# Optimization experiments

Hardware: AMD Instinct MI355X
Metric: run time of the kernel (lower is better)

## Reference

```python
import jax, jax.numpy as jnp
import numpy as np

B, L, D, N = 8, 1024, 1024, 32  # N = d_state // 2 (complex conjugate-pair modes)
DT_MIN, DT_MAX = 0.001, 0.1


def setup_inputs() -> dict:
    key = jax.random.key(0)
    ks = jax.random.split(key, 12)
    s = 1.0 / np.sqrt(D)  # torch Linear / Conv1d default init bound
    inp = {
        "x": jax.random.normal(ks[0], (B, L, D), jnp.float32),
        "in_W": jax.random.uniform(ks[1], (D, D), jnp.float32, -s, s),
        "in_b": jax.random.uniform(ks[2], (D,), jnp.float32, -s, s),
        # S4D kernel params
        "log_dt": (np.log(DT_MIN)
                   + jax.random.uniform(ks[3], (D,), jnp.float32)
                   * (np.log(DT_MAX) - np.log(DT_MIN))).astype(jnp.float32),
        "C": jax.random.normal(ks[4], (D, N, 2), jnp.float32),  # complex C as (re, im)
        "log_A_real": jnp.log(0.5 * jnp.ones((D, N), jnp.float32)),
        "A_imag": jnp.tile((np.pi * jnp.arange(N, dtype=np.float32))[None, :], (D, 1)),
        "D_skip": jax.random.normal(ks[5], (D,), jnp.float32),
        # output_linear = Conv1d(D, 2D, 1) + GLU(dim=-2); kernel squeezed to (2D, D)
        "glu_W": jax.random.uniform(ks[6], (2 * D, D), jnp.float32, -s, s),
        "glu_b": jax.random.uniform(ks[7], (2 * D,), jnp.float32, -s, s),
        "out_W": jax.random.uniform(ks[8], (D, D), jnp.float32, -s, s),
        "out_b": jax.random.uniform(ks[9], (D,), jnp.float32, -s, s),
    }
    return inp


def reference(x, in_W, in_b, log_dt, C, log_A_real, A_imag, D_skip,
              glu_W, glu_b, out_W, out_b):
    # in_proj
    x_in = x @ in_W.T + in_b                      # (B, L, D)
    u = jnp.swapaxes(x_in, 1, 2)                  # (B, D, L) -- transposed=False path
    Lseq = u.shape[-1]

    # ---- S4D kernel (ZOH-like discretization of diagonal SSM) ----
    dt = jnp.exp(log_dt)                          # (D,)
    Cc = (C[..., 0] + 1j * C[..., 1]).astype(jnp.complex64)   # (D, N)
    A = (-jnp.exp(log_A_real) + 1j * A_imag).astype(jnp.complex64)
    dtA = A * dt[:, None].astype(jnp.complex64)   # (D, N)
    # Vandermonde: exp(dtA * l) for l in [0, L)
    K = jnp.exp(dtA[:, :, None] * jnp.arange(Lseq, dtype=jnp.float32))  # (D, N, L)
    Ceff = Cc * (jnp.exp(dtA) - 1.0) / A
    k = 2.0 * jnp.einsum('hn,hnl->hl', Ceff, K).real            # (D, L)

    # ---- FFT causal convolution ----
    n = 2 * Lseq
    k_f = jnp.fft.rfft(k, n=n)                    # (D, L+1)
    u_f = jnp.fft.rfft(u, n=n)                    # (B, D, L+1)
    y = jnp.fft.irfft(u_f * k_f, n=n)[..., :Lseq] # (B, D, L)

    y = y + u * D_skip[:, None]                   # skip connection
    y = jax.nn.gelu(y, approximate=False)         # torch nn.GELU (erf)

    # Conv1d(D, 2D, kernel=1) + GLU over channel dim
    z = jnp.einsum('oh,bhl->bol', glu_W, y) + glu_b[None, :, None]
    a, g = jnp.split(z, 2, axis=1)
    y = a * jax.nn.sigmoid(g)                     # (B, D, L)

    y = jnp.swapaxes(y, 1, 2)                     # (B, L, D)
    out = y @ out_W.T + out_b
    return out + x
```

## Files before the change

### kernel.cpp

```cpp
#include <hip/hip_runtime.h>
#include <math.h>

#define BB 8
#define LL 1024
#define DD 1024
#define KD 1024
#define NM 32
#define NCH 16
#define CL 64
#define NTOK (BB * LL)
#define GSMEM 147456

typedef __bf16 bf16_t;
typedef __bf16 bf16x8 __attribute__((ext_vector_type(8)));
typedef __bf16 bf16x4 __attribute__((ext_vector_type(4)));
typedef float  f32x4  __attribute__((ext_vector_type(4)));

__device__ __forceinline__ float gelu_f(float z)
{
    float t = fmaf(0.044715f * z * z, z, z);
    return z / (1.f + expf(-1.5957691216f * t));
}

__global__ __launch_bounds__(256)
void f2b_all_kernel(const float* __restrict__ x,    bf16_t* __restrict__ xb,
                    const float* __restrict__ w0,   bf16_t* __restrict__ d0,
                    const float* __restrict__ w1,   bf16_t* __restrict__ d1,
                    const float* __restrict__ w2,   bf16_t* __restrict__ d2)
{
    int b = blockIdx.x;
    const float* s; bf16_t* d; int base;
    if (b < 8192)       { s = x;  d = xb; base = b; }
    else if (b < 9216)  { s = w0; d = d0; base = b - 8192; }
    else if (b < 11264) { s = w1; d = d1; base = b - 9216; }
    else                { s = w2; d = d2; base = b - 11264; }
    int i = (base * 256 + threadIdx.x) * 4;
    float4 f = *(const float4*)(s + i);
    bf16x4 o = { (bf16_t)f.x, (bf16_t)f.y, (bf16_t)f.z, (bf16_t)f.w };
    *(bf16x4*)(d + i) = o;
}

__device__ __forceinline__ void stage_tile(const bf16_t* __restrict__ Ag,
                                           const bf16_t* __restrict__ Bg,
                                           bf16_t* Asb, bf16_t* Bsb, int tid)
{
    #pragma unroll
    for (int p = 0; p < 4; ++p) {
        int e = p * 512 + tid;
        int row = e >> 3, c8 = (e & 7) << 3;
        int sc = c8 ^ ((row & 7) << 3);
        __builtin_amdgcn_global_load_lds(
            (const __attribute__((address_space(1))) void*)(Ag + (size_t)row * KD + sc),
            (__attribute__((address_space(3))) void*)(Asb + e * 8), 16, 0, 0);
    }
    #pragma unroll
    for (int p = 0; p < 2; ++p) {
        int e = p * 512 + tid;
        int row = e >> 3, c8 = (e & 7) << 3;
        int sc = c8 ^ ((row & 7) << 3);
        __builtin_amdgcn_global_load_lds(
            (const __attribute__((address_space(1))) void*)(Bg + (size_t)row * KD + sc),
            (__attribute__((address_space(3))) void*)(Bsb + e * 8), 16, 0, 0);
    }
}

__device__ __forceinline__ void compute_tile(const bf16_t* Asb, const bf16_t* Bsb,
                                             int wy, int wx, int lm, int ks,
                                             f32x4 (&acc)[4][4])
{
    #pragma unroll
    for (int kk = 0; kk < 2; ++kk) {
        bf16x8 af[4], bfr[4];
        const int col = kk * 32 + ks;
        #pragma unroll
        for (int i = 0; i < 4; ++i) {
            int row = wy * 64 + i * 16 + lm;
            af[i] = *(const bf16x8*)(Asb + row * 64 + (col ^ ((row & 7) << 3)));
        }
        #pragma unroll
        for (int j = 0; j < 4; ++j) {
            int row = wx * 64 + j * 16 + lm;
            bfr[j] = *(const bf16x8*)(Bsb + row * 64 + (col ^ ((row & 7) << 3)));
        }
        __builtin_amdgcn_s_setprio(1);
        #pragma unroll
        for (int i = 0; i < 4; ++i)
            #pragma unroll
            for (int j = 0; j < 4; ++j)
                acc[i][j] = __builtin_amdgcn_mfma_f32_16x16x32_bf16(
                                af[i], bfr[j], acc[i][j], 0, 0, 0);
        __builtin_amdgcn_s_setprio(0);
    }
}

template<int MODE>
__global__ __launch_bounds__(512, 2)
void gemm3_kernel(const bf16_t* __restrict__ A, const bf16_t* __restrict__ B,
                  const float* __restrict__ bias, const float* __restrict__ res,
                  void* __restrict__ outp)
{
    extern __shared__ __align__(16) bf16_t lds[];
    bf16_t* As0 = lds;
    bf16_t* Bs0 = lds + 3 * 16384;

    const int tid = threadIdx.x;
    const int lane = tid & 63, w = tid >> 6;
    const int wy = w >> 1, wx = w & 1;
    const int lm = lane & 15, ks = (lane >> 4) << 3;

    const int nbx = gridDim.x;
    int bid = blockIdx.y * nbx + blockIdx.x;
    const int cpx = (gridDim.x * gridDim.y) >> 3;
    bid = (bid & 7) * cpx + (bid >> 3);
    const int by = bid / nbx, bx = bid % nbx;
    const int m0 = by * 256, n0 = bx * 128;

    const bf16_t* Ag     = A + (size_t)m0 * KD;
    const bf16_t* Bbase0 = B + (size_t)n0 * KD;
    const bf16_t* Bbase1 = (MODE == 1) ? B + (size_t)(1024 + n0) * KD : Bbase0;
    const int NTT = (MODE == 1) ? 32 : 16;

    f32x4 acc[4][4]  = {};
    f32x4 acc2[4][4] = {};

    stage_tile(Ag,      Bbase0,      As0,         Bs0,        tid);
    stage_tile(Ag + 64, Bbase0 + 64, As0 + 16384, Bs0 + 8192, tid);
    asm volatile("s_waitcnt vmcnt(6)" ::: "memory");
    __builtin_amdgcn_s_barrier();

    #pragma unroll 1
    for (int t = 0; t < NTT; ++t) {
        if (t + 2 < NTT) {
            int q2 = (t + 2) % 3;
            const bf16_t* Agt = Ag + ((t + 2) & 15) * 64;
            const bf16_t* Bgt = ((MODE == 1 && t + 2 >= 16) ? Bbase1 : Bbase0)
                                + ((t + 2) & 15) * 64;
            stage_tile(Agt, Bgt, As0 + q2 * 16384, Bs0 + q2 * 8192, tid);
        }
        int q = t % 3;
        if (MODE == 1 && t >= 16)
            compute_tile(As0 + q * 16384, Bs0 + q * 8192, wy, wx, lm, ks, acc2);
        else
            compute_tile(As0 + q * 16384, Bs0 + q * 8192, wy, wx, lm, ks, acc);
        if (t + 1 < NTT) {
            if (t + 2 < NTT) asm volatile("s_waitcnt vmcnt(6) lgkmcnt(0)" ::: "memory");
            else             asm volatile("s_waitcnt vmcnt(0) lgkmcnt(0)" ::: "memory");
            __builtin_amdgcn_s_barrier();
        }
    }

    const int r4 = (lane >> 4) << 2;
    #pragma unroll
    for (int i = 0; i < 4; ++i)
        #pragma unroll
        for (int r = 0; r < 4; ++r) {
            int m = m0 + wy * 64 + i * 16 + r4 + r;
            #pragma unroll
            for (int j = 0; j < 4; ++j) {
                int n = n0 + wx * 64 + j * 16 + lm;
                if (MODE == 0) {
                    ((bf16_t*)outp)[(size_t)m * 8192 + n] =
                        (bf16_t)(acc[i][j][r] + bias[m]);
                } else if (MODE == 1) {
                    float a = acc[i][j][r]  + bias[n];
                    float g = acc2[i][j][r] + bias[1024 + n];
                    ((bf16_t*)outp)[(size_t)m * 1024 + n] =
                        (bf16_t)(a / (1.f + expf(-g)));
                } else {
                    ((float*)outp)[(size_t)m * 1024 + n] =
                        acc[i][j][r] + bias[n] + res[(size_t)m * 1024 + n];
                }
            }
        }
}

__global__ __launch_bounds__(64)
void genVTP_kernel(const float* __restrict__ log_dt, const float* __restrict__ lar,
                   const float* __restrict__ aim, const float* __restrict__ Cp,
                   const float* __restrict__ dskip,
                   bf16_t* __restrict__ V, bf16_t* __restrict__ TP)
{
    const int tid = threadIdx.x;
    if (blockIdx.x < DD / 2) {
        const int h = blockIdx.x * 2 + (tid >> 5);
        const int n = tid & 31;
        const float dt = expf(log_dt[h]);
        const float ardt = -expf(lar[h * NM + n]) * dt;
        const float aidt = aim[h * NM + n] * dt;
        float sn, cs;
        sincosf(aidt, &sn, &cs);
        float er = expf(ardt);
        float wr = er * cs, wi = er * sn;
        float inv = 1.f / fmaf(wr, wr, wi * wi);
        float vr = wr * inv, vi = -wi * inv;
        sincosf(63.f * aidt, &sn, &cs);
        er = expf(63.f * ardt);
        float pr = er * cs, pi = er * sn;
        bf16_t* rowr = V + ((size_t)h * 64 + 2 * n) * 64;
        bf16_t* rowi = rowr + 64;
        #pragma unroll
        for (int c8 = 0; c8 < 8; ++c8) {
            bf16x8 rr, ri;
            #pragma unroll
            for (int e = 0; e < 8; ++e) {
                rr[e] = (bf16_t)pr; ri[e] = (bf16_t)pi;
                float t = fmaf(pr, vr, -pi * vi);
                pi = fmaf(pr, vi, pi * vr);
                pr = t;
            }
            *(bf16x8*)(rowr + c8 * 8) = rr;
            *(bf16x8*)(rowi + c8 * 8) = ri;
        }
        return;
    }
    __shared__ float ardt_s[NM], aidt_s[NM], cr_s[NM], ci_s[NM], K_s[CL];
    const int h = blockIdx.x - DD / 2;
    const float dt = expf(log_dt[h]);
    if (tid < NM) {
        int n = tid;
        float ar = -expf(lar[h * NM + n]);
        float ai = aim[h * NM + n];
        float sn, cs;
        sincosf(ai * dt, &sn, &cs);
        float er = expf(ar * dt);
        float wrr = er * cs, wii = er * sn;
        float Crr = Cp[(h * NM + n) * 2 + 0];
        float Cii = Cp[(h * NM + n) * 2 + 1];
        float nr = fmaf(Crr, wrr - 1.f, -Cii * wii);
        float ni = fmaf(Crr, wii, Cii * (wrr - 1.f));
        float inv = 2.f / fmaf(ar, ar, ai * ai);
        cr_s[n] = fmaf(nr, ar, ni * ai) * inv;
        ci_s[n] = fmaf(ni, ar, -nr * ai) * inv;
        ardt_s[n] = ar * dt;
        aidt_s[n] = ai * dt;
    }
    __syncthreads();
    {
        float d = (float)tid;
        float kv = (tid == 0) ? dskip[h] : 0.f;
        #pragma unroll 8
        for (int n = 0; n < NM; ++n) {
            float sn, cs;
            sincosf(aidt_s[n] * d, &sn, &cs);
            float e = expf(ardt_s[n] * d);
            kv = fmaf(cr_s[n], e * cs, kv);
            kv = fmaf(-ci_s[n], e * sn, kv);
        }
        K_s[tid] = kv;
    }
    __syncthreads();
    const int i = tid;
    bf16_t* row = TP + ((size_t)h * CL + i) * 128;
    #pragma unroll
    for (int c8 = 0; c8 < 8; ++c8) {
        bf16x8 v;
        #pragma unroll
        for (int e = 0; e < 8; ++e) {
            int l = c8 * 8 + e;
            v[e] = (l <= i) ? (bf16_t)K_s[i - l] : (bf16_t)0.f;
        }
        *(bf16x8*)(row + c8 * 8) = v;
    }
    const float fi = (float)(i + 1);
    #pragma unroll
    for (int c8 = 0; c8 < 8; ++c8) {
        bf16x8 v;
        #pragma unroll
        for (int q = 0; q < 4; ++q) {
            int n = c8 * 4 + q;
            float sn, cs;
            sincosf(aidt_s[n] * fi, &sn, &cs);
            float e = expf(ardt_s[n] * fi);
            float Wr = e * cs, Wi = e * sn;
            v[2 * q]     = (bf16_t)(fmaf(cr_s[n], Wr, -ci_s[n] * Wi));
            v[2 * q + 1] = (bf16_t)(-fmaf(cr_s[n], Wi, ci_s[n] * Wr));
        }
        *(bf16x8*)(row + 64 + c8 * 8) = v;
    }
}

__global__ __launch_bounds__(256)
void ssm_fused_kernel(const bf16_t* __restrict__ u_ch, const bf16_t* __restrict__ V,
                      const bf16_t* __restrict__ TP,
                      const float* __restrict__ log_dt, const float* __restrict__ lar,
                      const float* __restrict__ aim, bf16_t* __restrict__ y_bi)
{
    __shared__ float  Sbc_s[128 * 64];
    __shared__ bf16_t Sc_s[128 * 64];
    const int h = blockIdx.x;
    const int tid = threadIdx.x;
    const int lane = tid & 63, w = tid >> 6;
    const int lm = lane & 15, ks = (lane >> 4) << 3;
    const bf16_t* U   = u_ch + (size_t)h * 8192;
    const bf16_t* Vh  = V    + (size_t)h * 4096;
    const bf16_t* TPh = TP   + (size_t)h * 8192;

    bf16x8 af_u[2][2];
    #pragma unroll
    for (int im = 0; im < 2; ++im)
        #pragma unroll
        for (int kk = 0; kk < 2; ++kk)
            af_u[im][kk] = *(const bf16x8*)(U + (((w << 1) + im) * 16 + lm) * 64
                                            + kk * 32 + ks);

    f32x4 acc1[2][4] = {};
    #pragma unroll
    for (int kk = 0; kk < 2; ++kk) {
        bf16x8 bfr[4];
        #pragma unroll
        for (int jn = 0; jn < 4; ++jn)
            bfr[jn] = *(const bf16x8*)(Vh + (jn * 16 + lm) * 64 + kk * 32 + ks);
        #pragma unroll
        for (int im = 0; im < 2; ++im)
            #pragma unroll
            for (int jn = 0; jn < 4; ++jn)
                acc1[im][jn] = __builtin_amdgcn_mfma_f32_16x16x32_bf16(
                                   af_u[im][kk], bfr[jn], acc1[im][jn], 0, 0, 0);
    }
    const int r4 = (lane >> 4) << 2;
    #pragma unroll
    for (int im = 0; im < 2; ++im)
        #pragma unroll
        for (int jn = 0; jn < 4; ++jn)
            #pragma unroll
            for (int r = 0; r < 4; ++r)
                Sbc_s[(((w << 1) + im) * 16 + r4 + r) * 64 + jn * 16 + lm]
                    = acc1[im][jn][r];
    __syncthreads();

    {
        const int b = tid >> 5, n = tid & 31;
        const float dtv = expf(log_dt[h]);
        const float ardt = -expf(lar[h * NM + n]) * dtv;
        const float aidt = aim[h * NM + n] * dtv;
        float sn, cs;
        sincosf(64.f * aidt, &sn, &cs);
        float er = expf(64.f * ardt);
        const float gr = er * cs, gi = er * sn;
        float sr = 0.f, si = 0.f;
        for (int c = 0; c < NCH; ++c) {
            int idx = (b * 16 + c) * 64 + 2 * n;
            float lr = Sbc_s[idx], li = Sbc_s[idx + 1];
            Sc_s[idx]     = (bf16_t)sr;
            Sc_s[idx + 1] = (bf16_t)si;
            float t0 = fmaf(gr, sr, fmaf(-gi, si, lr));
            si = fmaf(gr, si, fmaf(gi, sr, li));
            sr = t0;
        }
    }
    __syncthreads();

    f32x4 acc2[2][4] = {};
    #pragma unroll
    for (int kk = 0; kk < 4; ++kk) {
        bf16x8 af[2], bfr[4];
        #pragma unroll
        for (int im = 0; im < 2; ++im) {
            if (kk < 2)
                af[im] = af_u[im][kk];
            else
                af[im] = *(bf16x8*)&Sc_s[(((w << 1) + im) * 16 + lm) * 64
                                         + (kk - 2) * 32 + ks];
        }
        #pragma unroll
        for (int jn = 0; jn < 4; ++jn)
            bfr[jn] = *(const bf16x8*)(TPh + (jn * 16 + lm) * 128 + kk * 32 + ks);
        #pragma unroll
        for (int im = 0; im < 2; ++im)
            #pragma unroll
            for (int jn = 0; jn < 4; ++jn)
                acc2[im][jn] = __builtin_amdgcn_mfma_f32_16x16x32_bf16(
                                   af[im], bfr[jn], acc2[im][jn], 0, 0, 0);
    }
    bf16_t* out = y_bi + (size_t)h * 8192;
    #pragma unroll
    for (int im = 0; im < 2; ++im)
        #pragma unroll
        for (int jn = 0; jn < 4; ++jn)
            #pragma unroll
            for (int r = 0; r < 4; ++r) {
                int batch = ((w << 1) + im) * 16 + r4 + r;
                int i = jn * 16 + lm;
                out[batch * 64 + i] = (bf16_t)gelu_f(acc2[im][jn][r]);
            }
}

__global__ __launch_bounds__(256)
void transpose_kernel(const bf16_t* __restrict__ src, bf16_t* __restrict__ dst,
                      int src_rows, int src_cols)
{
    __shared__ unsigned short tile[64][68];
    const int tid = threadIdx.x;
    const int c0 = blockIdx.x << 6, r0 = blockIdx.y << 6;
    const int r = tid >> 4, c4 = (tid & 15) << 2;
    #pragma unroll
    for (int p = 0; p < 4; ++p) {
        int rr = p * 16 + r;
        ushort4 v = *(const ushort4*)((const unsigned short*)src +
                                      (size_t)(r0 + rr) * src_cols + c0 + c4);
        *(ushort4*)&tile[rr][c4] = v;
    }
    __syncthreads();
    #pragma unroll
    for (int p = 0; p < 4; ++p) {
        int rr = p * 16 + r;
        ushort4 v;
        v.x = tile[c4 + 0][rr];
        v.y = tile[c4 + 1][rr];
        v.z = tile[c4 + 2][rr];
        v.w = tile[c4 + 3][rr];
        *(ushort4*)((unsigned short*)dst + (size_t)(c0 + rr) * src_rows + r0 + c4) = v;
    }
}

extern "C" void kernel_launch(void* const* d_in, const int* in_sizes, int n_in,
                              void* d_out, int out_size, void* d_ws, size_t ws_size,
                              hipStream_t stream)
{
    (void)in_sizes; (void)n_in; (void)out_size; (void)ws_size;
    const float* x      = (const float*)d_in[0];
    const float* in_W   = (const float*)d_in[1];
    const float* in_b   = (const float*)d_in[2];
    const float* log_dt = (const float*)d_in[3];
    const float* Cp     = (const float*)d_in[4];
    const float* lar    = (const float*)d_in[5];
    const float* aim    = (const float*)d_in[6];
    const float* dsk    = (const float*)d_in[7];
    const float* gluW   = (const float*)d_in[8];
    const float* glub   = (const float*)d_in[9];
    const float* outW   = (const float*)d_in[10];
    const float* outb   = (const float*)d_in[11];

    char* ws = (char*)d_ws;
    bf16_t* xb    = (bf16_t*)(ws);
    bf16_t* TP    = (bf16_t*)(ws);
    bf16_t* y_tok = (bf16_t*)(ws);
    bf16_t* V     = (bf16_t*)(ws + 16777216);
    bf16_t* vb    = (bf16_t*)(ws + 16777216);
    bf16_t* u_ch  = (bf16_t*)(ws + 33554432);
    bf16_t* wbin  = (bf16_t*)(ws + 50331648);
    bf16_t* wbglu = (bf16_t*)(ws + 52428800);
    bf16_t* wbout = (bf16_t*)(ws + 56623104);
    bf16_t* y_bi  = (bf16_t*)d_out;

    static bool s_attr = false;
    if (!s_attr) {
        hipFuncSetAttribute((const void*)gemm3_kernel<0>,
                            hipFuncAttributeMaxDynamicSharedMemorySize, GSMEM);
        hipFuncSetAttribute((const void*)gemm3_kernel<1>,
                            hipFuncAttributeMaxDynamicSharedMemorySize, GSMEM);
        hipFuncSetAttribute((const void*)gemm3_kernel<2>,
                            hipFuncAttributeMaxDynamicSharedMemorySize, GSMEM);
        s_attr = true;
    }

    f2b_all_kernel<<<dim3(12288), dim3(256), 0, stream>>>(
        x, xb, in_W, wbin, gluW, wbglu, outW, wbout);

    gemm3_kernel<0><<<dim3(NTOK / 128, DD / 256), dim3(512), GSMEM, stream>>>(
        wbin, xb, in_b, nullptr, u_ch);

    genVTP_kernel<<<dim3(DD / 2 + DD), dim3(64), 0, stream>>>(
        log_dt, lar, aim, Cp, dsk, V, TP);
    ssm_fused_kernel<<<dim3(DD), dim3(256), 0, stream>>>(
        u_ch, V, TP, log_dt, lar, aim, y_bi);

    transpose_kernel<<<dim3(NTOK / 64, DD / 64), dim3(256), 0, stream>>>(y_bi, y_tok, DD, NTOK);
    gemm3_kernel<1><<<dim3(1024 / 128, NTOK / 256), dim3(512), GSMEM, stream>>>(
        y_tok, wbglu, glub, nullptr, vb);

    gemm3_kernel<2><<<dim3(DD / 128, NTOK / 256), dim3(512), GSMEM, stream>>>(
        vb, wbout, outb, x, d_out);
}
```

Before: 293.0 us.

## Interleave GEMM tile prefetch with MFMA phases using split barriers

```diff
diff --git a/kernel.cpp b/kernel.cpp
--- a/kernel.cpp
+++ b/kernel.cpp
@@ -40,68 +40,39 @@
     *(bf16x4*)(d + i) = o;
 }
 
-__device__ __forceinline__ void stage_tile(const bf16_t* __restrict__ Ag,
-                                           const bf16_t* __restrict__ Bg,
-                                           bf16_t* Asb, bf16_t* Bsb, int tid)
-{
-    #pragma unroll
-    for (int p = 0; p < 4; ++p) {
-        int e = p * 512 + tid;
+#define GLL(gp, lp) __builtin_amdgcn_global_load_lds( \
+    (const __attribute__((address_space(1))) void*)(gp), \
+    (__attribute__((address_space(3))) void*)(lp), 16, 0, 0)
+
+__device__ __forceinline__ void stage_chunk(const bf16_t* __restrict__ Ag,
+                                            const bf16_t* __restrict__ Bg,
+                                            bf16_t* Asb, bf16_t* Bsb,
+                                            int h, int tid)
+{
+    #pragma unroll
+    for (int q = 0; q < 2; ++q) {
+        int e = (h * 2 + q) * 512 + tid;
         int row = e >> 3, c8 = (e & 7) << 3;
         int sc = c8 ^ ((row & 7) << 3);
-        __builtin_amdgcn_global_load_lds(
-            (const __attribute__((address_space(1))) void*)(Ag + (size_t)row * KD + sc),
-            (__attribute__((address_space(3))) void*)(Asb + e * 8), 16, 0, 0);
-    }
-    #pragma unroll
-    for (int p = 0; p < 2; ++p) {
-        int e = p * 512 + tid;
+        GLL(Ag + (size_t)row * KD + sc, Asb + e * 8);
+    }
+    {
+        int e = h * 512 + tid;
         int row = e >> 3, c8 = (e & 7) << 3;
         int sc = c8 ^ ((row & 7) << 3);
-        __builtin_amdgcn_global_load_lds(
-            (const __attribute__((address_space(1))) void*)(Bg + (size_t)row * KD + sc),
-            (__attribute__((address_space(3))) void*)(Bsb + e * 8), 16, 0, 0);
-    }
-}
-
-__device__ __forceinline__ void compute_tile(const bf16_t* Asb, const bf16_t* Bsb,
-                                             int wy, int wx, int lm, int ks,
-                                             f32x4 (&acc)[4][4])
-{
-    #pragma unroll
-    for (int kk = 0; kk < 2; ++kk) {
-        bf16x8 af[4], bfr[4];
-        const int col = kk * 32 + ks;
-        #pragma unroll
-        for (int i = 0; i < 4; ++i) {
-            int row = wy * 64 + i * 16 + lm;
-            af[i] = *(const bf16x8*)(Asb + row * 64 + (col ^ ((row & 7) << 3)));
-        }
-        #pragma unroll
-        for (int j = 0; j < 4; ++j) {
-            int row = wx * 64 + j * 16 + lm;
-            bfr[j] = *(const bf16x8*)(Bsb + row * 64 + (col ^ ((row & 7) << 3)));
-        }
-        __builtin_amdgcn_s_setprio(1);
-        #pragma unroll
-        for (int i = 0; i < 4; ++i)
-            #pragma unroll
-            for (int j = 0; j < 4; ++j)
-                acc[i][j] = __builtin_amdgcn_mfma_f32_16x16x32_bf16(
-                                af[i], bfr[j], acc[i][j], 0, 0, 0);
-        __builtin_amdgcn_s_setprio(0);
+        GLL(Bg + (size_t)row * KD + sc, Bsb + e * 8);
     }
 }
 
 template<int MODE>
 __global__ __launch_bounds__(512, 2)
-void gemm3_kernel(const bf16_t* __restrict__ A, const bf16_t* __restrict__ B,
-                  const float* __restrict__ bias, const float* __restrict__ res,
-                  void* __restrict__ outp)
+void gemm8p_kernel(const bf16_t* __restrict__ A, const bf16_t* __restrict__ B,
+                   const float* __restrict__ bias, const float* __restrict__ res,
+                   void* __restrict__ outp)
 {
     extern __shared__ __align__(16) bf16_t lds[];
-    bf16_t* As0 = lds;
-    bf16_t* Bs0 = lds + 3 * 16384;
+    bf16_t* As = lds;
+    bf16_t* Bs = lds + 3 * 16384;
 
     const int tid = threadIdx.x;
     const int lane = tid & 63, w = tid >> 6;
@@ -115,38 +86,73 @@
     const int by = bid / nbx, bx = bid % nbx;
     const int m0 = by * 256, n0 = bx * 128;
 
-    const bf16_t* Ag     = A + (size_t)m0 * KD;
-    const bf16_t* Bbase0 = B + (size_t)n0 * KD;
-    const bf16_t* Bbase1 = (MODE == 1) ? B + (size_t)(1024 + n0) * KD : Bbase0;
-    const int NTT = (MODE == 1) ? 32 : 16;
+    const bf16_t* Ag = A + (size_t)m0 * KD;
+    const bf16_t* B0 = B + (size_t)n0 * KD;
+    const bf16_t* B1 = (MODE == 1) ? B + (size_t)(1024 + n0) * KD : B0;
+    const int NT = (MODE == 1) ? 32 : 16;
 
     f32x4 acc[4][4]  = {};
     f32x4 acc2[4][4] = {};
 
-    stage_tile(Ag,      Bbase0,      As0,         Bs0,        tid);
-    stage_tile(Ag + 64, Bbase0 + 64, As0 + 16384, Bs0 + 8192, tid);
+    stage_chunk(Ag,      B0,      As,         Bs,        0, tid);
+    stage_chunk(Ag,      B0,      As,         Bs,        1, tid);
+    stage_chunk(Ag + 64, B0 + 64, As + 16384, Bs + 8192, 0, tid);
+    stage_chunk(Ag + 64, B0 + 64, As + 16384, Bs + 8192, 1, tid);
     asm volatile("s_waitcnt vmcnt(6)" ::: "memory");
     __builtin_amdgcn_s_barrier();
 
     #pragma unroll 1
-    for (int t = 0; t < NTT; ++t) {
-        if (t + 2 < NTT) {
-            int q2 = (t + 2) % 3;
-            const bf16_t* Agt = Ag + ((t + 2) & 15) * 64;
-            const bf16_t* Bgt = ((MODE == 1 && t + 2 >= 16) ? Bbase1 : Bbase0)
-                                + ((t + 2) & 15) * 64;
-            stage_tile(Agt, Bgt, As0 + q2 * 16384, Bs0 + q2 * 8192, tid);
-        }
-        int q = t % 3;
-        if (MODE == 1 && t >= 16)
-            compute_tile(As0 + q * 16384, Bs0 + q * 8192, wy, wx, lm, ks, acc2);
-        else
-            compute_tile(As0 + q * 16384, Bs0 + q * 8192, wy, wx, lm, ks, acc);
-        if (t + 1 < NTT) {
-            if (t + 2 < NTT) asm volatile("s_waitcnt vmcnt(6) lgkmcnt(0)" ::: "memory");
-            else             asm volatile("s_waitcnt vmcnt(0) lgkmcnt(0)" ::: "memory");
-            __builtin_amdgcn_s_barrier();
-        }
+    for (int t = 0; t < NT; ++t) {
+        const int q = t % 3;
+        const bf16_t* Asb = As + q * 16384;
+        const bf16_t* Bsb = Bs + q * 8192;
+        const int t2 = t + 2;
+        const bool st = (t2 < NT);
+        const bf16_t* Ag2 = Ag;
+        const bf16_t* Bg2 = B0;
+        bf16_t* As2 = As; bf16_t* Bs2 = Bs;
+        if (st) {
+            int q2 = t2 % 3;
+            Ag2 = Ag + (t2 & 15) * 64;
+            Bg2 = ((MODE == 1 && t2 >= 16) ? B1 : B0) + (t2 & 15) * 64;
+            As2 = As + q2 * 16384; Bs2 = Bs + q2 * 8192;
+        }
+
+        auto tile_body = [&](f32x4 (&ac)[4][4]) {
+            #pragma unroll
+            for (int kk = 0; kk < 2; ++kk) {
+                bf16x8 af[4], bfr[4];
+                const int col = kk * 32 + ks;
+                #pragma unroll
+                for (int i = 0; i < 4; ++i) {
+                    int row = wy * 64 + i * 16 + lm;
+                    af[i] = *(const bf16x8*)(Asb + row * 64
+                                             + (col ^ ((row & 7) << 3)));
+                }
+                #pragma unroll
+                for (int j = 0; j < 4; ++j) {
+                    int row = wx * 64 + j * 16 + lm;
+                    bfr[j] = *(const bf16x8*)(Bsb + row * 64
+                                              + (col ^ ((row & 7) << 3)));
+                }
+                if (st) stage_chunk(Ag2, Bg2, As2, Bs2, kk, tid);
+                __builtin_amdgcn_s_barrier();
+                __builtin_amdgcn_s_setprio(1);
+                #pragma unroll
+                for (int i = 0; i < 4; ++i)
+                    #pragma unroll
+                    for (int j = 0; j < 4; ++j)
+                        ac[i][j] = __builtin_amdgcn_mfma_f32_16x16x32_bf16(
+                                       af[i], bfr[j], ac[i][j], 0, 0, 0);
+                __builtin_amdgcn_s_setprio(0);
+                if (kk == 1 && t + 1 < NT) {
+                    if (st) asm volatile("s_waitcnt vmcnt(6)" ::: "memory");
+                    else    asm volatile("s_waitcnt vmcnt(0)" ::: "memory");
+                }
+                __builtin_amdgcn_s_barrier();
+            }
+        };
+        if (MODE == 1 && t >= 16) tile_body(acc2); else tile_body(acc);
     }
 
     const int r4 = (lane >> 4) << 2;
@@ -445,11 +451,11 @@
 
     static bool s_attr = false;
     if (!s_attr) {
-        hipFuncSetAttribute((const void*)gemm3_kernel<0>,
+        hipFuncSetAttribute((const void*)gemm8p_kernel<0>,
                             hipFuncAttributeMaxDynamicSharedMemorySize, GSMEM);
-        hipFuncSetAttribute((const void*)gemm3_kernel<1>,
+        hipFuncSetAttribute((const void*)gemm8p_kernel<1>,
                             hipFuncAttributeMaxDynamicSharedMemorySize, GSMEM);
-        hipFuncSetAttribute((const void*)gemm3_kernel<2>,
+        hipFuncSetAttribute((const void*)gemm8p_kernel<2>,
                             hipFuncAttributeMaxDynamicSharedMemorySize, GSMEM);
         s_attr = true;
     }
@@ -457,7 +463,7 @@
     f2b_all_kernel<<<dim3(12288), dim3(256), 0, stream>>>(
         x, xb, in_W, wbin, gluW, wbglu, outW, wbout);
 
-    gemm3_kernel<0><<<dim3(NTOK / 128, DD / 256), dim3(512), GSMEM, stream>>>(
+    gemm8p_kernel<0><<<dim3(NTOK / 128, DD / 256), dim3(512), GSMEM, stream>>>(
         wbin, xb, in_b, nullptr, u_ch);
 
     genVTP_kernel<<<dim3(DD / 2 + DD), dim3(64), 0, stream>>>(
@@ -466,9 +472,9 @@
         u_ch, V, TP, log_dt, lar, aim, y_bi);
 
     transpose_kernel<<<dim3(NTOK / 64, DD / 64), dim3(256), 0, stream>>>(y_bi, y_tok, DD, NTOK);
-    gemm3_kernel<1><<<dim3(1024 / 128, NTOK / 256), dim3(512), GSMEM, stream>>>(
+    gemm8p_kernel<1><<<dim3(1024 / 128, NTOK / 256), dim3(512), GSMEM, stream>>>(
         y_tok, wbglu, glub, nullptr, vb);
 
-    gemm3_kernel<2><<<dim3(DD / 128, NTOK / 256), dim3(512), GSMEM, stream>>>(
+    gemm8p_kernel<2><<<dim3(DD / 128, NTOK / 256), dim3(512), GSMEM, stream>>>(
         vb, wbout, outb, x, d_out);
 }
```

New measurement: 341.2 us. 1.16x slower.
